# Kernel tuning notes

Hardware: AMD Instinct MI355X
Metric: run time of the kernel (lower is better)

The kernel has to match this reference:

```python
import jax, jax.numpy as jnp
import numpy as np

N = 100000      # entity nodes
E = 1000000     # edges per relation
D_IN = 256
HID = 128
EPS = 1e-16     # PyG softmax denominator eps
NEG_SLOPE = 0.2 # GATConv default leaky_relu slope


def _gat_conv(x, ei, Ws, Wd, a_s, a_d, b):
    """Single-head GATConv (heads=1, concat=False) with self-loops."""
    n = x.shape[0]
    loop = jnp.arange(n, dtype=ei.dtype)
    src = jnp.concatenate([ei[0], loop])  # [E+N]
    dst = jnp.concatenate([ei[1], loop])
    h_src = x @ Ws                         # [N, HID]
    h_dst = x @ Wd                         # [N, HID]
    a_src = h_src @ a_s                    # [N]
    a_dst = h_dst @ a_d                    # [N]
    e = jax.nn.leaky_relu(a_src[src] + a_dst[dst], NEG_SLOPE)  # [E+N]
    # numerically-stable softmax over incoming edges of each dst node
    m = jax.ops.segment_max(e, dst, num_segments=n)
    ex = jnp.exp(e - m[dst])
    denom = jax.ops.segment_sum(ex, dst, num_segments=n)
    alpha = ex / (denom[dst] + EPS)        # [E+N]
    out = jax.ops.segment_sum(alpha[:, None] * h_src[src], dst, num_segments=n)
    return out + b


def setup_inputs() -> dict:
    key = jax.random.key(0)
    ks = jax.random.split(key, 9)
    s_in = 1.0 / np.sqrt(D_IN)
    s_h = 1.0 / np.sqrt(HID)
    return {
        "x": jax.random.normal(ks[0], (N, D_IN), dtype=jnp.float32),
        "edge_index_r0": jax.random.randint(ks[1], (2, E), 0, N, dtype=jnp.int64)
                         if jax.config.jax_enable_x64 else jax.random.randint(ks[1], (2, E), 0, N).astype(jnp.int32),
        "edge_index_r1": jax.random.randint(ks[2], (2, E), 0, N, dtype=jnp.int64)
                         if jax.config.jax_enable_x64 else jax.random.randint(ks[2], (2, E), 0, N).astype(jnp.int32),
        "W_src": jax.random.normal(ks[3], (2, D_IN, HID), dtype=jnp.float32) * s_in,
        "W_dst": jax.random.normal(ks[4], (2, D_IN, HID), dtype=jnp.float32) * s_in,
        "att_src": jax.random.normal(ks[5], (2, HID), dtype=jnp.float32) * s_h,
        "att_dst": jax.random.normal(ks[6], (2, HID), dtype=jnp.float32) * s_h,
        "bias": jnp.zeros((2, HID), dtype=jnp.float32),
    }


def reference(x, edge_index_r0, edge_index_r1, W_src, W_dst, att_src, att_dst, bias):
    # HeteroConv aggr='sum' over the two entity->entity relations
    out = _gat_conv(x, edge_index_r0, W_src[0], W_dst[0], att_src[0], att_dst[0], bias[0])
    out = out + _gat_conv(x, edge_index_r1, W_src[1], W_dst[1], att_src[1], att_dst[1], bias[1])
    # ELU; dropout p=0.0 is identity
    return jax.nn.elu(out)
```

## Files before the change

### kernel.cpp

```cpp
#include <hip/hip_runtime.h>

typedef __attribute__((ext_vector_type(8))) __bf16 bf16x8;
typedef __attribute__((ext_vector_type(4))) float floatx4;

__device__ __forceinline__ float bf2f(unsigned short u) {
    return __uint_as_float(((unsigned)u) << 16);
}
__device__ __forceinline__ unsigned short f2bf(float f) {
    unsigned u = __float_as_uint(f);
    unsigned r = u + 0x7FFFu + ((u >> 16) & 1u);
    return (unsigned short)(r >> 16);
}

__global__ void detect_k(const unsigned short* __restrict__ xs, int* __restrict__ flag) {
    __shared__ int sred[256];
    int tid = threadIdx.x;
    int cnt = 0;
    for (int j = 0; j < 16; ++j) {
        unsigned short u = xs[(tid * 16 + j) * 2];
        int e = (u >> 7) & 0xFF;
        cnt += (e >= 96 && e <= 159) ? 1 : 0;
    }
    sred[tid] = cnt;
    __syncthreads();
    for (int s = 128; s > 0; s >>= 1) {
        if (tid < s) sred[tid] += sred[tid + s];
        __syncthreads();
    }
    if (tid == 0) *flag = (sred[0] > 2048) ? 1 : 0;
}

__device__ __forceinline__ void canon8(const void* src, unsigned short* dst,
                                       long long idx, int f) {
    if (f) {
        *(uint4*)&dst[idx] = *(const uint4*)((const unsigned short*)src + idx);
    } else {
        const float* sf = (const float*)src;
        unsigned short v[8];
        for (int j = 0; j < 8; ++j) v[j] = f2bf(sf[idx + j]);
        *(uint4*)&dst[idx] = *(const uint4*)v;
    }
}

__global__ void canon5_k(const void* Ws, const void* Wd, const void* as,
                         const void* ad, const void* b,
                         unsigned short* Wsb, unsigned short* Wdb,
                         unsigned short* asb, unsigned short* adb,
                         unsigned short* bsb, const int* __restrict__ flag) {
    int blk = blockIdx.x, tid = threadIdx.x;
    int f = *flag;
    if (blk < 64) {
        const void* src = blk < 32 ? Ws : Wd;
        unsigned short* dst = blk < 32 ? Wsb : Wdb;
        long long idx = ((long long)(blk & 31) * 256 + tid) * 8;
        canon8(src, dst, idx, f);
    } else {
        if (tid < 32)       canon8(as, asb, (long long)tid * 8, f);
        else if (tid < 64)  canon8(ad, adb, (long long)(tid - 32) * 8, f);
        else if (tid < 96)  canon8(b,  bsb, (long long)(tid - 64) * 8, f);
    }
}

__global__ void vec_kernel(const unsigned short* __restrict__ Ws,
                           const unsigned short* __restrict__ Wd,
                           const unsigned short* __restrict__ as_,
                           const unsigned short* __restrict__ ad_,
                           float* __restrict__ vecs) {
    int r = blockIdx.x;
    int k = threadIdx.x;
    float s = 0.f, t = 0.f;
    const unsigned short* wsrow = Ws + (size_t)r * 32768 + (size_t)k * 128;
    const unsigned short* wdrow = Wd + (size_t)r * 32768 + (size_t)k * 128;
    for (int h = 0; h < 128; ++h) {
        s += bf2f(wsrow[h]) * bf2f(as_[r * 128 + h]);
        t += bf2f(wdrow[h]) * bf2f(ad_[r * 128 + h]);
    }
    vecs[(r * 2 + 0) * 256 + k] = s;
    vecs[(r * 2 + 1) * 256 + k] = t;
}

__global__ void transpose_W(const unsigned short* __restrict__ W,
                            unsigned short* __restrict__ Bt) {
    int i = blockIdx.x * 256 + threadIdx.x;
    if (i >= 2 * 256 * 128) return;
    int r = i >> 15, rem = i & 32767;
    int k = rem >> 7, n = rem & 127;
    Bt[(size_t)r * 32768 + n * 256 + k] = W[i];
}

__global__ __launch_bounds__(256) void a_canon_k(const void* __restrict__ xraw,
                                                 unsigned short* __restrict__ xb,
                                                 const float* __restrict__ vecs,
                                                 float* __restrict__ aout, int n,
                                                 const int* __restrict__ flag) {
    __shared__ float sv[1024];
    int tid = threadIdx.x;
    for (int j = 0; j < 4; ++j) sv[j * 256 + tid] = vecs[j * 256 + tid];
    __syncthreads();
    int lane = tid & 63, wave = tid >> 6;
    int row = blockIdx.x * 4 + wave;
    if (row >= n) return;
    float xf[4];
    if (*flag) {
        uint2 u = *(const uint2*)((const unsigned short*)xraw + (size_t)row * 256 + lane * 4);
        xf[0] = bf2f((unsigned short)(u.x & 0xFFFF));
        xf[1] = bf2f((unsigned short)(u.x >> 16));
        xf[2] = bf2f((unsigned short)(u.y & 0xFFFF));
        xf[3] = bf2f((unsigned short)(u.y >> 16));
        *(uint2*)&xb[(size_t)row * 256 + lane * 4] = u;
    } else {
        float4 f = *(const float4*)((const float*)xraw + (size_t)row * 256 + lane * 4);
        xf[0] = f.x; xf[1] = f.y; xf[2] = f.z; xf[3] = f.w;
        unsigned short v[4] = {f2bf(f.x), f2bf(f.y), f2bf(f.z), f2bf(f.w)};
        *(uint2*)&xb[(size_t)row * 256 + lane * 4] = *(const uint2*)v;
    }
    float s[4] = {0.f, 0.f, 0.f, 0.f};
    for (int j = 0; j < 4; ++j)
        for (int q = 0; q < 4; ++q)
            s[j] += xf[q] * sv[j * 256 + lane * 4 + q];
    for (int j = 0; j < 4; ++j)
        for (int off = 32; off > 0; off >>= 1)
            s[j] += __shfl_down(s[j], off);
    if (lane == 0)
        for (int j = 0; j < 4; ++j) aout[(size_t)j * n + row] = s[j];
}

__global__ __launch_bounds__(256) void gemm_h(const unsigned short* __restrict__ x,
                                              const unsigned short* __restrict__ Btg,
                                              unsigned short* __restrict__ hout, int n) {
    const int r = blockIdx.y;
    const unsigned short* bt = Btg + (size_t)r * 32768;
    unsigned short* h = hout + (size_t)r * n * 128;
    const int r0 = blockIdx.x * 128;
    __shared__ __align__(16) unsigned short As[128 * 40];
    __shared__ __align__(16) unsigned short Bs[128 * 40];
    int tid = threadIdx.x;
    int lane = tid & 63, wave = tid >> 6;

    floatx4 acc[2][8];
    for (int mt = 0; mt < 2; ++mt)
        for (int nt = 0; nt < 8; ++nt)
            acc[mt][nt] = (floatx4){0.f, 0.f, 0.f, 0.f};

    for (int k0 = 0; k0 < 256; k0 += 32) {
        for (int i = 0; i < 2; ++i) {
            int L = i * 256 + tid;
            int row = L >> 2, kc = (L & 3) * 8;
            uint4 va = make_uint4(0u, 0u, 0u, 0u);
            int gr = r0 + row;
            if (gr < n) va = *(const uint4*)&x[(size_t)gr * 256 + k0 + kc];
            *(uint4*)&As[row * 40 + kc] = va;
            uint4 vb = *(const uint4*)&bt[(size_t)row * 256 + k0 + kc];
            *(uint4*)&Bs[row * 40 + kc] = vb;
        }
        __syncthreads();
        int qk = (lane >> 4) * 8;
        int m16 = lane & 15;
        bf16x8 af[2], bfv[8];
        af[0] = *(const bf16x8*)&As[(wave * 32 + m16) * 40 + qk];
        af[1] = *(const bf16x8*)&As[(wave * 32 + 16 + m16) * 40 + qk];
        for (int nt = 0; nt < 8; ++nt)
            bfv[nt] = *(const bf16x8*)&Bs[(nt * 16 + m16) * 40 + qk];
        for (int mt = 0; mt < 2; ++mt)
            for (int nt = 0; nt < 8; ++nt)
                acc[mt][nt] = __builtin_amdgcn_mfma_f32_16x16x32_bf16(
                    af[mt], bfv[nt], acc[mt][nt], 0, 0, 0);
        __syncthreads();
    }
    int col0 = lane & 15;
    for (int mt = 0; mt < 2; ++mt) {
        int baser = r0 + wave * 32 + mt * 16 + (lane >> 4) * 4;
        for (int nt = 0; nt < 8; ++nt)
            for (int i = 0; i < 4; ++i) {
                int gr = baser + i;
                if (gr < n) h[(size_t)gr * 128 + nt * 16 + col0] = f2bf(acc[mt][nt][i]);
            }
    }
}

__global__ void hist2_k(const int* __restrict__ ei0, const int* __restrict__ ei1,
                        int* __restrict__ cnt0, int* __restrict__ cnt1,
                        int E_, int n) {
    int rel = blockIdx.y;
    const int* ei = rel ? ei1 : ei0;
    int* cnt = rel ? cnt1 : cnt0;
    int t = blockIdx.x * 256 + threadIdx.x;
    if (t >= E_ + n) return;
    int d = (t < E_) ? ei[E_ + t] : (t - E_);
    atomicAdd(&cnt[d], 1);
}

__global__ __launch_bounds__(256) void scan_red_k(const int* __restrict__ cnt0,
                                                  const int* __restrict__ cnt1,
                                                  int* __restrict__ part,
                                                  int n, int nb) {
    __shared__ int s[256];
    int rel = blockIdx.y;
    const int* cnt = rel ? cnt1 : cnt0;
    int i = blockIdx.x * 256 + threadIdx.x;
    s[threadIdx.x] = (i < n) ? cnt[i] : 0;
    __syncthreads();
    for (int o = 128; o > 0; o >>= 1) {
        if (threadIdx.x < o) s[threadIdx.x] += s[threadIdx.x + o];
        __syncthreads();
    }
    if (threadIdx.x == 0) part[rel * nb + blockIdx.x] = s[0];
}

__global__ __launch_bounds__(1024) void scan_mid_k(int* __restrict__ part, int nb) {
    __shared__ int s[1024];
    int rel = blockIdx.x;
    int t = threadIdx.x;
    s[t] = (t < nb) ? part[rel * nb + t] : 0;
    __syncthreads();
    for (int o = 1; o < 1024; o <<= 1) {
        int v = (t >= o) ? s[t - o] : 0;
        __syncthreads();
        s[t] += v;
        __syncthreads();
    }
    if (t < nb) part[rel * nb + t] = (t == 0) ? 0 : s[t - 1];
}

__global__ __launch_bounds__(256) void scan_off_k(const int* __restrict__ cnt0,
                                                  const int* __restrict__ cnt1,
                                                  const int* __restrict__ part,
                                                  int* __restrict__ off0,
                                                  int* __restrict__ off1,
                                                  int n, int nb) {
    __shared__ int s[256];
    int rel = blockIdx.y;
    const int* cnt = rel ? cnt1 : cnt0;
    int* off = rel ? off1 : off0;
    int i = blockIdx.x * 256 + threadIdx.x;
    int t = threadIdx.x;
    int v = (i < n) ? cnt[i] : 0;
    s[t] = v;
    __syncthreads();
    for (int o = 1; o < 256; o <<= 1) {
        int u = (t >= o) ? s[t - o] : 0;
        __syncthreads();
        s[t] += u;
        __syncthreads();
    }
    if (i < n) off[i] = part[rel * nb + blockIdx.x] + s[t] - v;
}

__global__ void fill2_k(const int* __restrict__ ei0, const int* __restrict__ ei1,
                        const float* __restrict__ avals,
                        int* __restrict__ off0, int* __restrict__ off1,
                        unsigned long long* __restrict__ pair0,
                        unsigned long long* __restrict__ pair1,
                        int E_, int n) {
    int rel = blockIdx.y;
    const int* ei = rel ? ei1 : ei0;
    const float* as_ = avals + (rel ? 2 * (size_t)n : 0);
    const float* ad_ = avals + (rel ? 3 * (size_t)n : (size_t)n);
    int* off = rel ? off1 : off0;
    unsigned long long* pair = rel ? pair1 : pair0;
    int t = blockIdx.x * 256 + threadIdx.x;
    if (t >= E_ + n) return;
    int s, d;
    if (t < E_) { s = ei[t]; d = ei[E_ + t]; } else { s = t - E_; d = s; }
    float e = as_[s] + ad_[d];
    e = e > 0.f ? e : 0.2f * e;
    int pos = atomicAdd(&off[d], 1);
    pair[pos] = ((unsigned long long)__float_as_uint(e) << 32) | (unsigned)s;
}

__device__ __forceinline__ void rel_acc4(int d, int g, int l, int lane,
                                         const int* __restrict__ off,
                                         const unsigned long long* __restrict__ pair,
                                         const unsigned short* __restrict__ h,
                                         float* __restrict__ o ) {
    int s0 = d ? off[d - 1] : 0;
    int e0 = off[d];
    float m = -1e30f;
    for (int i = s0 + lane; i < e0; i += 64)
        m = fmaxf(m, __uint_as_float((unsigned)(pair[i] >> 32)));
    for (int o_ = 1; o_ < 64; o_ <<= 1) m = fmaxf(m, __shfl_xor(m, o_));
    float denom = 0.f;
    float a[8] = {0.f, 0.f, 0.f, 0.f, 0.f, 0.f, 0.f, 0.f};
    for (int base = s0; base < e0; base += 4) {
        int i = base + g;
        if (i < e0) {
            unsigned long long pe = pair[i];
            int s = (int)(unsigned)pe;
            float ev = __uint_as_float((unsigned)(pe >> 32));
            float w = __expf(ev - m);
            denom += w;
            uint4 hv = *(const uint4*)&h[(size_t)s * 128 + l * 8];
            a[0] += w * bf2f((unsigned short)(hv.x & 0xFFFFu));
            a[1] += w * bf2f((unsigned short)(hv.x >> 16));
            a[2] += w * bf2f((unsigned short)(hv.y & 0xFFFFu));
            a[3] += w * bf2f((unsigned short)(hv.y >> 16));
            a[4] += w * bf2f((unsigned short)(hv.z & 0xFFFFu));
            a[5] += w * bf2f((unsigned short)(hv.z >> 16));
            a[6] += w * bf2f((unsigned short)(hv.w & 0xFFFFu));
            a[7] += w * bf2f((unsigned short)(hv.w >> 16));
        }
    }
    for (int j = 0; j < 8; ++j) {
        a[j] += __shfl_xor(a[j], 16);
        a[j] += __shfl_xor(a[j], 32);
    }
    denom += __shfl_xor(denom, 16);
    denom += __shfl_xor(denom, 32);
    float inv = 1.f / (denom + 1e-16f);
    for (int j = 0; j < 8; ++j) o[j] = a[j] * inv;
}

__global__ __launch_bounds__(256) void agg_k(
    const int* __restrict__ off0, const unsigned long long* __restrict__ pair0,
    const int* __restrict__ off1, const unsigned long long* __restrict__ pair1,
    const unsigned short* __restrict__ h0, const unsigned short* __restrict__ h1,
    const unsigned short* __restrict__ bias, void* __restrict__ out,
    int n, const int* __restrict__ flag) {
    int wave = threadIdx.x >> 6, lane = threadIdx.x & 63;
    int g = lane >> 4, l = lane & 15;
    int d = blockIdx.x * 4 + wave;
    if (d >= n) return;
    float p[8], q[8];
    rel_acc4(d, g, l, lane, off0, pair0, h0, p);
    rel_acc4(d, g, l, lane, off1, pair1, h1, q);
    uint4 b0 = *(const uint4*)&bias[l * 8];
    uint4 b1 = *(const uint4*)&bias[128 + l * 8];
    const unsigned* b0u = (const unsigned*)&b0;
    const unsigned* b1u = (const unsigned*)&b1;
    float v[8];
    for (int j = 0; j < 8; ++j) {
        unsigned w0 = b0u[j >> 1], w1 = b1u[j >> 1];
        float bb = bf2f((unsigned short)((j & 1) ? (w0 >> 16) : (w0 & 0xFFFFu)))
                 + bf2f((unsigned short)((j & 1) ? (w1 >> 16) : (w1 & 0xFFFFu)));
        float t = p[j] + q[j] + bb;
        v[j] = t > 0.f ? t : (__expf(t) - 1.f);
    }
    if (g == 0) {
        if (*flag) {
            unsigned pk[4];
            for (int j = 0; j < 4; ++j)
                pk[j] = ((unsigned)f2bf(v[2 * j + 1]) << 16) | (unsigned)f2bf(v[2 * j]);
            ((uint4*)out)[(size_t)d * 16 + l] = *(const uint4*)pk;
        } else {
            float4 f0 = make_float4(v[0], v[1], v[2], v[3]);
            float4 f1 = make_float4(v[4], v[5], v[6], v[7]);
            ((float4*)out)[(size_t)d * 32 + l * 2] = f0;
            ((float4*)out)[(size_t)d * 32 + l * 2 + 1] = f1;
        }
    }
}

static inline char* carve(char*& p, size_t bytes) {
    char* r = p;
    p += (bytes + 255) & ~(size_t)255;
    return r;
}

extern "C" void kernel_launch(void* const* d_in, const int* in_sizes, int n_in,
                              void* d_out, int out_size, void* d_ws, size_t ws_size,
                              hipStream_t stream) {
    (void)n_in; (void)out_size; (void)ws_size;
    const void* x_raw  = d_in[0];
    const int*  ei0    = (const int*)d_in[1];
    const int*  ei1    = (const int*)d_in[2];
    const void* Ws_raw = d_in[3];
    const void* Wd_raw = d_in[4];
    const void* as_raw = d_in[5];
    const void* ad_raw = d_in[6];
    const void* b_raw  = d_in[7];

    const int n = in_sizes[0] / 256;
    const int e = in_sizes[1] / 2;
    const int tot = e + n;
    const int nb = (n + 255) / 256;

    char* p = (char*)d_ws;
    float* avals = (float*)carve(p, (size_t)4 * n * 4);
    int*   cnt0  = (int*)carve(p, (size_t)2 * n * 4);
    int*   cnt1  = cnt0 + n;
    int*   off0  = (int*)carve(p, (size_t)n * 4);
    int*   off1  = (int*)carve(p, (size_t)n * 4);
    int*   part  = (int*)carve(p, (size_t)2 * nb * 4);
    unsigned long long* pair0 = (unsigned long long*)carve(p, (size_t)tot * 8);
    unsigned long long* pair1 = (unsigned long long*)carve(p, (size_t)tot * 8);
    float* vecs  = (float*)carve(p, 1024 * 4);
    int*   flag  = (int*)carve(p, 256);
    unsigned short* xb  = (unsigned short*)carve(p, (size_t)n * 256 * 2);
    unsigned short* h0  = (unsigned short*)carve(p, (size_t)2 * n * 128 * 2);
    unsigned short* h1  = h0 + (size_t)n * 128;
    unsigned short* Wsb = (unsigned short*)carve(p, 65536 * 2);
    unsigned short* Wdb = (unsigned short*)carve(p, 65536 * 2);
    unsigned short* Bt  = (unsigned short*)carve(p, 65536 * 2);
    unsigned short* asb = (unsigned short*)carve(p, 256 * 2);
    unsigned short* adb = (unsigned short*)carve(p, 256 * 2);
    unsigned short* bsb = (unsigned short*)carve(p, 256 * 2);

    hipMemsetAsync(cnt0, 0, (size_t)2 * n * 4, stream);

    detect_k<<<1, 256, 0, stream>>>((const unsigned short*)x_raw, flag);
    canon5_k<<<65, 256, 0, stream>>>(Ws_raw, Wd_raw, as_raw, ad_raw, b_raw,
                                     Wsb, Wdb, asb, adb, bsb, flag);
    vec_kernel<<<2, 256, 0, stream>>>(Wsb, Wdb, asb, adb, vecs);
    transpose_W<<<(2 * 256 * 128 + 255) / 256, 256, 0, stream>>>(Wsb, Bt);

    int gb = (tot + 255) / 256;
    hist2_k<<<dim3(gb, 2), 256, 0, stream>>>(ei0, ei1, cnt0, cnt1, e, n);
    scan_red_k<<<dim3(nb, 2), 256, 0, stream>>>(cnt0, cnt1, part, n, nb);
    scan_mid_k<<<2, 1024, 0, stream>>>(part, nb);
    scan_off_k<<<dim3(nb, 2), 256, 0, stream>>>(cnt0, cnt1, part, off0, off1, n, nb);

    a_canon_k<<<(n + 3) / 4, 256, 0, stream>>>(x_raw, xb, vecs, avals, n, flag);
    gemm_h<<<dim3((n + 127) / 128, 2), 256, 0, stream>>>(xb, Bt, h0, n);

    fill2_k<<<dim3(gb, 2), 256, 0, stream>>>(ei0, ei1, avals, off0, off1,
                                             pair0, pair1, e, n);

    agg_k<<<(n + 3) / 4, 256, 0, stream>>>(off0, pair0, off1, pair1,
                                           h0, h1, bsb, d_out, n, flag);
}
```

Baseline: 541.5 us.

## Record per-edge rank in histogram to drop fill atomics; unroll aggregation loop

```diff
diff --git a/kernel.cpp b/kernel.cpp
--- a/kernel.cpp
+++ b/kernel.cpp
@@ -180,14 +180,16 @@
 
 __global__ void hist2_k(const int* __restrict__ ei0, const int* __restrict__ ei1,
                         int* __restrict__ cnt0, int* __restrict__ cnt1,
+                        int* __restrict__ rank0, int* __restrict__ rank1,
                         int E_, int n) {
     int rel = blockIdx.y;
     const int* ei = rel ? ei1 : ei0;
     int* cnt = rel ? cnt1 : cnt0;
+    int* rank = rel ? rank1 : rank0;
     int t = blockIdx.x * 256 + threadIdx.x;
     if (t >= E_ + n) return;
     int d = (t < E_) ? ei[E_ + t] : (t - E_);
-    atomicAdd(&cnt[d], 1);
+    rank[t] = atomicAdd(&cnt[d], 1);
 }
 
 __global__ __launch_bounds__(256) void scan_red_k(const int* __restrict__ cnt0,
@@ -248,7 +250,8 @@
 
 __global__ void fill2_k(const int* __restrict__ ei0, const int* __restrict__ ei1,
                         const float* __restrict__ avals,
-                        int* __restrict__ off0, int* __restrict__ off1,
+                        const int* __restrict__ off0, const int* __restrict__ off1,
+                        const int* __restrict__ rank0, const int* __restrict__ rank1,
                         unsigned long long* __restrict__ pair0,
                         unsigned long long* __restrict__ pair1,
                         int E_, int n) {
@@ -256,7 +259,8 @@
     const int* ei = rel ? ei1 : ei0;
     const float* as_ = avals + (rel ? 2 * (size_t)n : 0);
     const float* ad_ = avals + (rel ? 3 * (size_t)n : (size_t)n);
-    int* off = rel ? off1 : off0;
+    const int* off = rel ? off1 : off0;
+    const int* rank = rel ? rank1 : rank0;
     unsigned long long* pair = rel ? pair1 : pair0;
     int t = blockIdx.x * 256 + threadIdx.x;
     if (t >= E_ + n) return;
@@ -264,41 +268,52 @@
     if (t < E_) { s = ei[t]; d = ei[E_ + t]; } else { s = t - E_; d = s; }
     float e = as_[s] + ad_[d];
     e = e > 0.f ? e : 0.2f * e;
-    int pos = atomicAdd(&off[d], 1);
+    int pos = off[d] + rank[t];
     pair[pos] = ((unsigned long long)__float_as_uint(e) << 32) | (unsigned)s;
+}
+
+__device__ __forceinline__ void acc8(float* a, float w, const uint4& hv) {
+    a[0] += w * bf2f((unsigned short)(hv.x & 0xFFFFu));
+    a[1] += w * bf2f((unsigned short)(hv.x >> 16));
+    a[2] += w * bf2f((unsigned short)(hv.y & 0xFFFFu));
+    a[3] += w * bf2f((unsigned short)(hv.y >> 16));
+    a[4] += w * bf2f((unsigned short)(hv.z & 0xFFFFu));
+    a[5] += w * bf2f((unsigned short)(hv.z >> 16));
+    a[6] += w * bf2f((unsigned short)(hv.w & 0xFFFFu));
+    a[7] += w * bf2f((unsigned short)(hv.w >> 16));
 }
 
 __device__ __forceinline__ void rel_acc4(int d, int g, int l, int lane,
                                          const int* __restrict__ off,
+                                         const int* __restrict__ cnt,
                                          const unsigned long long* __restrict__ pair,
                                          const unsigned short* __restrict__ h,
                                          float* __restrict__ o ) {
-    int s0 = d ? off[d - 1] : 0;
-    int e0 = off[d];
+    int s0 = off[d];
+    int e0 = s0 + cnt[d];
     float m = -1e30f;
     for (int i = s0 + lane; i < e0; i += 64)
         m = fmaxf(m, __uint_as_float((unsigned)(pair[i] >> 32)));
     for (int o_ = 1; o_ < 64; o_ <<= 1) m = fmaxf(m, __shfl_xor(m, o_));
     float denom = 0.f;
     float a[8] = {0.f, 0.f, 0.f, 0.f, 0.f, 0.f, 0.f, 0.f};
-    for (int base = s0; base < e0; base += 4) {
-        int i = base + g;
-        if (i < e0) {
-            unsigned long long pe = pair[i];
-            int s = (int)(unsigned)pe;
-            float ev = __uint_as_float((unsigned)(pe >> 32));
-            float w = __expf(ev - m);
-            denom += w;
-            uint4 hv = *(const uint4*)&h[(size_t)s * 128 + l * 8];
-            a[0] += w * bf2f((unsigned short)(hv.x & 0xFFFFu));
-            a[1] += w * bf2f((unsigned short)(hv.x >> 16));
-            a[2] += w * bf2f((unsigned short)(hv.y & 0xFFFFu));
-            a[3] += w * bf2f((unsigned short)(hv.y >> 16));
-            a[4] += w * bf2f((unsigned short)(hv.z & 0xFFFFu));
-            a[5] += w * bf2f((unsigned short)(hv.z >> 16));
-            a[6] += w * bf2f((unsigned short)(hv.w & 0xFFFFu));
-            a[7] += w * bf2f((unsigned short)(hv.w >> 16));
-        }
+    int last = e0 - 1;
+    for (int base = s0; base < e0; base += 8) {
+        int i0 = base + g, i1 = i0 + 4;
+        int j0 = min(i0, last), j1 = min(i1, last);
+        unsigned long long p0 = pair[j0];
+        unsigned long long p1 = pair[j1];
+        int sA = (int)(unsigned)p0;
+        int sB = (int)(unsigned)p1;
+        uint4 hv0 = *(const uint4*)&h[(size_t)sA * 128 + l * 8];
+        uint4 hv1 = *(const uint4*)&h[(size_t)sB * 128 + l * 8];
+        float w0 = __expf(__uint_as_float((unsigned)(p0 >> 32)) - m);
+        float w1 = __expf(__uint_as_float((unsigned)(p1 >> 32)) - m);
+        w0 = (i0 < e0) ? w0 : 0.f;
+        w1 = (i1 < e0) ? w1 : 0.f;
+        denom += w0 + w1;
+        acc8(a, w0, hv0);
+        acc8(a, w1, hv1);
     }
     for (int j = 0; j < 8; ++j) {
         a[j] += __shfl_xor(a[j], 16);
@@ -311,8 +326,10 @@
 }
 
 __global__ __launch_bounds__(256) void agg_k(
-    const int* __restrict__ off0, const unsigned long long* __restrict__ pair0,
-    const int* __restrict__ off1, const unsigned long long* __restrict__ pair1,
+    const int* __restrict__ off0, const int* __restrict__ cnt0,
+    const unsigned long long* __restrict__ pair0,
+    const int* __restrict__ off1, const int* __restrict__ cnt1,
+    const unsigned long long* __restrict__ pair1,
     const unsigned short* __restrict__ h0, const unsigned short* __restrict__ h1,
     const unsigned short* __restrict__ bias, void* __restrict__ out,
     int n, const int* __restrict__ flag) {
@@ -321,8 +338,8 @@
     int d = blockIdx.x * 4 + wave;
     if (d >= n) return;
     float p[8], q[8];
-    rel_acc4(d, g, l, lane, off0, pair0, h0, p);
-    rel_acc4(d, g, l, lane, off1, pair1, h1, q);
+    rel_acc4(d, g, l, lane, off0, cnt0, pair0, h0, p);
+    rel_acc4(d, g, l, lane, off1, cnt1, pair1, h1, q);
     uint4 b0 = *(const uint4*)&bias[l * 8];
     uint4 b1 = *(const uint4*)&bias[128 + l * 8];
     const unsigned* b0u = (const unsigned*)&b0;
@@ -381,6 +398,8 @@
     int*   off0  = (int*)carve(p, (size_t)n * 4);
     int*   off1  = (int*)carve(p, (size_t)n * 4);
     int*   part  = (int*)carve(p, (size_t)2 * nb * 4);
+    int*   rank0 = (int*)carve(p, (size_t)tot * 4);
+    int*   rank1 = (int*)carve(p, (size_t)tot * 4);
     unsigned long long* pair0 = (unsigned long long*)carve(p, (size_t)tot * 8);
     unsigned long long* pair1 = (unsigned long long*)carve(p, (size_t)tot * 8);
     float* vecs  = (float*)carve(p, 1024 * 4);
@@ -404,7 +423,7 @@
     transpose_W<<<(2 * 256 * 128 + 255) / 256, 256, 0, stream>>>(Wsb, Bt);
 
     int gb = (tot + 255) / 256;
-    hist2_k<<<dim3(gb, 2), 256, 0, stream>>>(ei0, ei1, cnt0, cnt1, e, n);
+    hist2_k<<<dim3(gb, 2), 256, 0, stream>>>(ei0, ei1, cnt0, cnt1, rank0, rank1, e, n);
     scan_red_k<<<dim3(nb, 2), 256, 0, stream>>>(cnt0, cnt1, part, n, nb);
     scan_mid_k<<<2, 1024, 0, stream>>>(part, nb);
     scan_off_k<<<dim3(nb, 2), 256, 0, stream>>>(cnt0, cnt1, part, off0, off1, n, nb);
@@ -413,8 +432,8 @@
     gemm_h<<<dim3((n + 127) / 128, 2), 256, 0, stream>>>(xb, Bt, h0, n);
 
     fill2_k<<<dim3(gb, 2), 256, 0, stream>>>(ei0, ei1, avals, off0, off1,
-                                             pair0, pair1, e, n);
-
-    agg_k<<<(n + 3) / 4, 256, 0, stream>>>(off0, pair0, off1, pair1,
+                                             rank0, rank1, pair0, pair1, e, n);
+
+    agg_k<<<(n + 3) / 4, 256, 0, stream>>>(off0, cnt0, pair0, off1, cnt1, pair1,
                                            h0, h1, bsb, d_out, n, flag);
 }
```

Measured after the change: 500.6 us. 1.08x faster.
